# Performance work log

Hardware: AMD Instinct MI355X
Metric: run time of the kernel (lower is better)

The kernel has to match this reference:

```python
import jax, jax.numpy as jnp
import numpy as np

N, IN_F, OUT_F, H = 4096, 256, 64, 8

def setup_inputs() -> dict:
    key = jax.random.key(0)
    k1, k2, k3, k4 = jax.random.split(key, 4)
    x = jax.random.normal(k1, (N, IN_F), dtype=jnp.float32)
    adj = jax.random.randint(k2, (N, N), 0, 2, dtype=jnp.int32)
    # Xavier-uniform-ish init scale for params
    W = jax.random.uniform(k3, (H, IN_F, OUT_F), dtype=jnp.float32, minval=-1.0, maxval=1.0) * np.sqrt(6.0 / (IN_F + OUT_F))
    a = jax.random.uniform(k4, (H, 2 * OUT_F, 1), dtype=jnp.float32, minval=-1.0, maxval=1.0) * np.sqrt(6.0 / (2 * OUT_F + 1))
    return {"x": x, "adj": adj, "W": W, "a": a}

def reference(x, adj, W, a):
    # h: (H, N, F) per-head projected features
    h = jnp.einsum('nf,hfo->hno', x, W)
    F = h.shape[-1]
    # Decompose concat-score: [h_i || h_j] @ a == h_i @ a[:F] + h_j @ a[F:]
    a_src = a[:, :F, 0]   # (H, F)
    a_dst = a[:, F:, 0]   # (H, F)
    src = jnp.einsum('hno,ho->hn', h, a_src)  # (H, N)
    dst = jnp.einsum('hno,ho->hn', h, a_dst)  # (H, N)
    e = jax.nn.leaky_relu(src[:, :, None] + dst[:, None, :], negative_slope=0.2)  # (H, N, N)
    e = jnp.where(adj[None, :, :] == 0, -jnp.inf, e)
    alpha = jax.nn.softmax(e, axis=2)  # dropout is identity at eval
    h_prime = jnp.einsum('hnm,hmo->hno', alpha, h).mean(axis=0)  # (N, F)
    return jax.nn.elu(h_prime)
```

## Files before the change

kernel.cpp:

```cpp
#include <hip/hip_runtime.h>
#include <hip/hip_fp16.h>
#include <cstdint>

#define N_NODES 4096
#define IN_FEAT 256
#define OUT_FEAT 64
#define NHEAD 8
#define LOG2E 1.4426950408889634f

typedef _Float16 f16;
typedef f16   f16x2 __attribute__((ext_vector_type(2)));
typedef f16   f16x8 __attribute__((ext_vector_type(8)));
typedef float f32x4 __attribute__((ext_vector_type(4)));

#define OFF_SRCPK 4194304
#define OFF_DSTE1 4325376
#define OFF_DSTE5 4390912
#define OFF_WT    4456448
#define OFF_EM    4718592
#define OFF_NUMA  21495808ULL
#define OFF_DENA  29884416ULL

union HU { unsigned u; f16x2 h; };
union A8 { f16x8 v; unsigned u[4]; };

__device__ __forceinline__ void async_copy16(const void* g, void* l) {
    __builtin_amdgcn_global_load_lds(
        (const __attribute__((address_space(1))) void*)g,
        (__attribute__((address_space(3))) void*)l, 16, 0, 0);
}

static __device__ inline unsigned pkh2(float a, float b) {
    union { f16 h[2]; unsigned u; } t;
    t.h[0] = (f16)a; t.h[1] = (f16)b; return t.u;
}

__global__ __launch_bounds__(256) void gat_pack(
    const int* __restrict__ adj, unsigned* __restrict__ em32,
    const float* __restrict__ W, f16* __restrict__ Wt,
    float* __restrict__ zeroBase)
{
    if (blockIdx.x >= 1088) {
        size_t off = ((size_t)(blockIdx.x - 1088) * 256 + threadIdx.x) * 8;
        float4 z = {0.f, 0.f, 0.f, 0.f};
        *(float4*)(zeroBase + off)     = z;
        *(float4*)(zeroBase + off + 4) = z;
        return;
    }
    if (blockIdx.x >= 1024) {
        int gid = (blockIdx.x - 1024) * 256 + threadIdx.x;
        int hd  = gid >> 11;
        int rem = gid & 2047;
        int c   = rem >> 5;
        int kg  = rem & 31;
        const float* src = W + ((size_t)hd * IN_FEAT + kg * 8) * OUT_FEAT + c;
        f16x8 v;
        #pragma unroll
        for (int t = 0; t < 8; ++t) v[t] = (f16)src[(size_t)t * OUT_FEAT];
        *(f16x8*)(Wt + ((size_t)hd * OUT_FEAT + c) * IN_FEAT + kg * 8) = v;
        return;
    }

    const int wv   = threadIdx.x >> 6;
    const int lane = threadIdx.x & 63;
    const int row  = blockIdx.x * 4 + wv;
    const int* p   = adj + (size_t)row * N_NODES;
    unsigned* dst  = em32 + (size_t)row * (N_NODES / 4);
    #pragma unroll 4
    for (int s = 0; s < 16; ++s) {
        int4 v = *(const int4*)(p + s * 256 + lane * 4);
        unsigned d = (v.x ? 0x000000FFu : 0u) | (v.y ? 0x0000FF00u : 0u)
                   | (v.z ? 0x00FF0000u : 0u) | (v.w ? 0xFF000000u : 0u);
        dst[s * 64 + lane] = d;
    }
}

__global__ __launch_bounds__(256, 4) void gat_phase1(
    const float* __restrict__ x,
    const f16*   __restrict__ Wt,
    const float* __restrict__ a,
    f16*      __restrict__ h_t,
    unsigned* __restrict__ srcPK,
    f16*      __restrict__ dstE1,
    f16*      __restrict__ dstE5)
{
    __shared__ f16 xs[16][264];

    const int lane = threadIdx.x & 63;
    const int wv   = threadIdx.x >> 6;
    const int tile = blockIdx.x >> 1;
    const int hd   = (blockIdx.x & 1) * 4 + wv;
    const int r    = lane & 15;
    const int q    = lane >> 4;
    const int nb   = tile * 16;

    #pragma unroll
    for (int c = 0; c < 4; ++c) {
        int idx = c * 1024 + threadIdx.x * 4;
        int row = idx >> 8, col = idx & 255;
        float4 v = *(const float4*)(x + (size_t)(nb + row) * IN_FEAT + col);
        uint2 st = { pkh2(v.x, v.y), pkh2(v.z, v.w) };
        *(uint2*)(&xs[row][col]) = st;
    }
    __syncthreads();

    const f16* Wth = Wt + (size_t)hd * OUT_FEAT * IN_FEAT;
    f32x4 acc[4] = {};

    #pragma unroll 2
    for (int k0 = 0; k0 < IN_FEAT; k0 += 32) {
        f16x8 af = *(const f16x8*)(&xs[r][k0 + q * 8]);
        #pragma unroll
        for (int f = 0; f < 4; ++f) {
            f16x8 bf = *(const f16x8*)(Wth + (size_t)(16 * f + r) * IN_FEAT + k0 + q * 8);
            acc[f] = __builtin_amdgcn_mfma_f32_16x16x32_f16(af, bf, acc[f], 0, 0, 0);
        }
    }

    float asv[4], adv[4];
    #pragma unroll
    for (int f = 0; f < 4; ++f) {
        asv[f] = a[hd * 128 + 16 * f + r];
        adv[f] = a[hd * 128 + 64 + 16 * f + r];
    }
    float sp[4], dp[4];
    #pragma unroll
    for (int reg = 0; reg < 4; ++reg) {
        sp[reg] = acc[0][reg] * asv[0] + acc[1][reg] * asv[1]
                + acc[2][reg] * asv[2] + acc[3][reg] * asv[3];
        dp[reg] = acc[0][reg] * adv[0] + acc[1][reg] * adv[1]
                + acc[2][reg] * adv[2] + acc[3][reg] * adv[3];
    }
    #pragma unroll
    for (int m = 1; m <= 8; m <<= 1) {
        #pragma unroll
        for (int reg = 0; reg < 4; ++reg) {
            sp[reg] += __shfl_xor(sp[reg], m);
            dp[reg] += __shfl_xor(dp[reg], m);
        }
    }

    #pragma unroll
    for (int f = 0; f < 4; ++f) {
        uint2 st = { pkh2(acc[f][0], acc[f][1]), pkh2(acc[f][2], acc[f][3]) };
        *(uint2*)(h_t + (size_t)(hd * OUT_FEAT + 16 * f + r) * N_NODES + nb + 4 * q) = st;
    }

    if (r == 0) {
        #pragma unroll
        for (int reg = 0; reg < 4; ++reg) {
            int row = nb + 4 * q + reg;
            float s = sp[reg] * LOG2E;
            float d = dp[reg] * LOG2E;
            srcPK[hd * N_NODES + row] = pkh2(exp2f(s), exp2f(0.2f * s));
            dstE1[hd * N_NODES + row] = (f16)exp2f(d);
            dstE5[hd * N_NODES + row] = (f16)exp2f(0.2f * d);
        }
    }
}

__global__ __launch_bounds__(256, 4) void gat_phase2p(
    const f16* __restrict__ h_t,
    const unsigned* __restrict__ srcPK,
    const f16* __restrict__ dstE1,
    const f16* __restrict__ dstE5,
    const unsigned char* __restrict__ emask8,
    float* __restrict__ numA,
    float* __restrict__ denA)
{
    __shared__ f16 Vbuf[2][8320];

    const int t    = threadIdx.x;
    const int lane = t & 63;
    const int wv   = t >> 6;
    const int r    = lane & 15;
    const int q    = lane >> 4;
    const int q8   = q * 8;

    const int hd     = blockIdx.x >> 7;
    const int rowgrp = (blockIdx.x >> 2) & 31;
    const int chunk  = blockIdx.x & 3;
    const int nblk   = rowgrp * 128;
    const int n0     = nblk + wv * 32;
    const int mbase  = chunk * 1024;

    HU s0u, s1u;
    s0u.u = srcPK[hd * N_NODES + n0 + r];
    s1u.u = srcPK[hd * N_NODES + n0 + 16 + r];
    const f16x2 se1_0 = { s0u.h[0], s0u.h[0] };
    const f16x2 se5_0 = { s0u.h[1], s0u.h[1] };
    const f16x2 se1_1 = { s1u.h[0], s1u.h[0] };
    const f16x2 se5_1 = { s1u.h[1], s1u.h[1] };

    const f16* Vhead = h_t + (size_t)hd * OUT_FEAT * N_NODES + mbase;
    const f16* srcV  = Vhead + (size_t)(t >> 2) * N_NODES + (t & 3) * 8;
    const unsigned char* srcM =
        emask8 + (size_t)(nblk + (t >> 1)) * N_NODES + mbase + (t & 1) * 16;
    const f16* ebase = ((t >> 2) & 1) ? dstE5 : dstE1;
    const f16* esrc  = ebase + (size_t)hd * N_NODES + mbase
                             + (t >> 3) * 32 + (t & 3) * 8;

    f32x4 acc0 = {}, acc1 = {}, acc2 = {}, acc3 = {}, accD0 = {};
    f32x4 acc4 = {}, acc5 = {}, acc6 = {}, acc7 = {}, accD1 = {};
    f16x8 ones;
    #pragma unroll
    for (int j = 0; j < 8; ++j) ones[j] = (f16)1.0f;

    auto stage = [&](int buf, int it) {
        const int c64 = it * 64;
        async_copy16(srcV + c64,      &Vbuf[buf][t * 8]);
        async_copy16(srcV + c64 + 32, &Vbuf[buf][2048 + t * 8]);
        async_copy16(srcM + c64,      &Vbuf[buf][4096 + t * 8]);
        async_copy16(srcM + c64 + 32, &Vbuf[buf][6144 + t * 8]);
        if (t < 16) async_copy16(esrc + c64, &Vbuf[buf][8192 + t * 8]);
    };

    stage(0, 0);

    for (int it = 0; it < 16; ++it) {
        const int cur = it & 1;
        __syncthreads();

        stage(1 - cur, (it + 1) & 15);

        #pragma unroll
        for (int s = 0; s < 2; ++s) {
            const int vb = s * 2048;
            uint4 e1v = *(const uint4*)(&Vbuf[cur][8192 + s * 64 + q8]);
            uint4 e5v = *(const uint4*)(&Vbuf[cur][8224 + s * 64 + q8]);
            uint2 m0v = *(const uint2*)(&Vbuf[cur][4096 + s * 2048 + (wv * 32 + r) * 16 + q * 4]);
            uint2 m1v = *(const uint2*)(&Vbuf[cur][4096 + s * 2048 + (wv * 32 + 16 + r) * 16 + q * 4]);

            unsigned e1d[4] = {e1v.x, e1v.y, e1v.z, e1v.w};
            unsigned e5d[4] = {e5v.x, e5v.y, e5v.z, e5v.w};
            unsigned mk0[4], mk1[4];
            mk0[0] = __builtin_amdgcn_perm(0u, m0v.x, 0x01010000u);
            mk0[1] = __builtin_amdgcn_perm(0u, m0v.x, 0x03030202u);
            mk0[2] = __builtin_amdgcn_perm(0u, m0v.y, 0x01010000u);
            mk0[3] = __builtin_amdgcn_perm(0u, m0v.y, 0x03030202u);
            mk1[0] = __builtin_amdgcn_perm(0u, m1v.x, 0x01010000u);
            mk1[1] = __builtin_amdgcn_perm(0u, m1v.x, 0x03030202u);
            mk1[2] = __builtin_amdgcn_perm(0u, m1v.y, 0x01010000u);
            mk1[3] = __builtin_amdgcn_perm(0u, m1v.y, 0x03030202u);

            A8 A0, A1;
            #pragma unroll
            for (int jp = 0; jp < 4; ++jp) {
                HU ed1; ed1.u = e1d[jp];
                HU ed5; ed5.u = e5d[jp];
                HU w0, w1;
                w0.h = __builtin_elementwise_max(se1_0 * ed1.h, se5_0 * ed5.h);
                w1.h = __builtin_elementwise_max(se1_1 * ed1.h, se5_1 * ed5.h);
                A0.u[jp] = w0.u & mk0[jp];
                A1.u[jp] = w1.u & mk1[jp];
            }

            f16x8 b0 = *(const f16x8*)(&Vbuf[cur][vb + (     r) * 32 + q8]);
            f16x8 b1 = *(const f16x8*)(&Vbuf[cur][vb + (16 + r) * 32 + q8]);
            f16x8 b2 = *(const f16x8*)(&Vbuf[cur][vb + (32 + r) * 32 + q8]);
            f16x8 b3 = *(const f16x8*)(&Vbuf[cur][vb + (48 + r) * 32 + q8]);

            acc0  = __builtin_amdgcn_mfma_f32_16x16x32_f16(A0.v, b0,   acc0,  0, 0, 0);
            acc1  = __builtin_amdgcn_mfma_f32_16x16x32_f16(A0.v, b1,   acc1,  0, 0, 0);
            acc2  = __builtin_amdgcn_mfma_f32_16x16x32_f16(A0.v, b2,   acc2,  0, 0, 0);
            acc3  = __builtin_amdgcn_mfma_f32_16x16x32_f16(A0.v, b3,   acc3,  0, 0, 0);
            accD0 = __builtin_amdgcn_mfma_f32_16x16x32_f16(A0.v, ones, accD0, 0, 0, 0);
            acc4  = __builtin_amdgcn_mfma_f32_16x16x32_f16(A1.v, b0,   acc4,  0, 0, 0);
            acc5  = __builtin_amdgcn_mfma_f32_16x16x32_f16(A1.v, b1,   acc5,  0, 0, 0);
            acc6  = __builtin_amdgcn_mfma_f32_16x16x32_f16(A1.v, b2,   acc6,  0, 0, 0);
            acc7  = __builtin_amdgcn_mfma_f32_16x16x32_f16(A1.v, b3,   acc7,  0, 0, 0);
            accD1 = __builtin_amdgcn_mfma_f32_16x16x32_f16(A1.v, ones, accD1, 0, 0, 0);
        }
    }

    #pragma unroll
    for (int reg = 0; reg < 4; ++reg) {
        int row0 = n0 + 4 * q + reg;
        int row1 = row0 + 16;
        atomicAdd(&numA[((size_t)row0 * NHEAD + hd) * 64 +  0 + r], acc0[reg]);
        atomicAdd(&numA[((size_t)row0 * NHEAD + hd) * 64 + 16 + r], acc1[reg]);
        atomicAdd(&numA[((size_t)row0 * NHEAD + hd) * 64 + 32 + r], acc2[reg]);
        atomicAdd(&numA[((size_t)row0 * NHEAD + hd) * 64 + 48 + r], acc3[reg]);
        atomicAdd(&numA[((size_t)row1 * NHEAD + hd) * 64 +  0 + r], acc4[reg]);
        atomicAdd(&numA[((size_t)row1 * NHEAD + hd) * 64 + 16 + r], acc5[reg]);
        atomicAdd(&numA[((size_t)row1 * NHEAD + hd) * 64 + 32 + r], acc6[reg]);
        atomicAdd(&numA[((size_t)row1 * NHEAD + hd) * 64 + 48 + r], acc7[reg]);
        if (r == 0) {
            atomicAdd(&denA[(size_t)row0 * NHEAD + hd], accD0[reg]);
            atomicAdd(&denA[(size_t)row1 * NHEAD + hd], accD1[reg]);
        }
    }
}

__global__ __launch_bounds__(512) void gat_combine(
    const float* __restrict__ numA,
    const float* __restrict__ denA,
    float* __restrict__ out)
{
    int gid = blockIdx.x * 512 + threadIdx.x;
    int row = gid >> 5;
    int cp  = (gid & 31) * 2;
    float s0 = 0.f, s1 = 0.f;
    #pragma unroll
    for (int h = 0; h < NHEAD; ++h) {
        float2 v = *(const float2*)(numA + ((size_t)row * NHEAD + h) * 64 + cp);
        float inv = 1.f / denA[(size_t)row * NHEAD + h];
        s0 += v.x * inv;
        s1 += v.y * inv;
    }
    s0 *= 0.125f; s1 *= 0.125f;
    float e0 = s0 > 0.f ? s0 : expm1f(s0);
    float e1 = s1 > 0.f ? s1 : expm1f(s1);
    float2 pk = {e0, e1};
    *(float2*)(out + (size_t)row * OUT_FEAT + cp) = pk;
}

extern "C" void kernel_launch(void* const* d_in, const int* in_sizes, int n_in,
                              void* d_out, int out_size, void* d_ws, size_t ws_size,
                              hipStream_t stream)
{
    const float* x   = (const float*)d_in[0];
    const int*   adj = (const int*)d_in[1];
    const float* W   = (const float*)d_in[2];
    const float* a   = (const float*)d_in[3];
    float* out = (float*)d_out;

    char* ws = (char*)d_ws;
    f16*           h_t   = (f16*)ws;
    unsigned*      srcPK = (unsigned*)(ws + OFF_SRCPK);
    f16*           dstE1 = (f16*)(ws + OFF_DSTE1);
    f16*           dstE5 = (f16*)(ws + OFF_DSTE5);
    f16*           Wt    = (f16*)(ws + OFF_WT);
    unsigned char* em    = (unsigned char*)(ws + OFF_EM);
    float*         numA  = (float*)(ws + OFF_NUMA);
    float*         denA  = (float*)(ws + OFF_DENA);

    gat_pack   <<<2128, 256, 0, stream>>>(adj, (unsigned*)em, W, Wt, numA);
    gat_phase1 <<<512,  256, 0, stream>>>(x, Wt, a, h_t, srcPK, dstE1, dstE5);
    gat_phase2p<<<1024, 256, 0, stream>>>(h_t, srcPK, dstE1, dstE5, em, numA, denA);
    gat_combine<<<256,  512, 0, stream>>>(numA, denA, out);
}
```

Baseline: 172.1 us.

## Merge pack and projection kernels, read fp32 W directly in MFMA loop

Fuses the adjacency packing, accumulator zeroing and per-head projection into a single launch, so the separate W transpose/convert pass and its workspace are gone. The projection blocks now gather and convert W from fp32 directly inside the MFMA loop using strided scalar loads. This removes one kernel launch and one dependency boundary, and lets the projection overlap with the bandwidth-bound adjacency packing. The cost is uncoalesced global reads of W, repeated across tiles.

```diff
diff --git a/kernel.cpp b/kernel.cpp
--- a/kernel.cpp
+++ b/kernel.cpp
@@ -16,7 +16,6 @@
 #define OFF_SRCPK 4194304
 #define OFF_DSTE1 4325376
 #define OFF_DSTE5 4390912
-#define OFF_WT    4456448
 #define OFF_EM    4718592
 #define OFF_NUMA  21495808ULL
 #define OFF_DENA  29884416ULL
@@ -35,49 +34,12 @@
     t.h[0] = (f16)a; t.h[1] = (f16)b; return t.u;
 }
 
-__global__ __launch_bounds__(256) void gat_pack(
-    const int* __restrict__ adj, unsigned* __restrict__ em32,
-    const float* __restrict__ W, f16* __restrict__ Wt,
-    float* __restrict__ zeroBase)
-{
-    if (blockIdx.x >= 1088) {
-        size_t off = ((size_t)(blockIdx.x - 1088) * 256 + threadIdx.x) * 8;
-        float4 z = {0.f, 0.f, 0.f, 0.f};
-        *(float4*)(zeroBase + off)     = z;
-        *(float4*)(zeroBase + off + 4) = z;
-        return;
-    }
-    if (blockIdx.x >= 1024) {
-        int gid = (blockIdx.x - 1024) * 256 + threadIdx.x;
-        int hd  = gid >> 11;
-        int rem = gid & 2047;
-        int c   = rem >> 5;
-        int kg  = rem & 31;
-        const float* src = W + ((size_t)hd * IN_FEAT + kg * 8) * OUT_FEAT + c;
-        f16x8 v;
-        #pragma unroll
-        for (int t = 0; t < 8; ++t) v[t] = (f16)src[(size_t)t * OUT_FEAT];
-        *(f16x8*)(Wt + ((size_t)hd * OUT_FEAT + c) * IN_FEAT + kg * 8) = v;
-        return;
-    }
-
-    const int wv   = threadIdx.x >> 6;
-    const int lane = threadIdx.x & 63;
-    const int row  = blockIdx.x * 4 + wv;
-    const int* p   = adj + (size_t)row * N_NODES;
-    unsigned* dst  = em32 + (size_t)row * (N_NODES / 4);
-    #pragma unroll 4
-    for (int s = 0; s < 16; ++s) {
-        int4 v = *(const int4*)(p + s * 256 + lane * 4);
-        unsigned d = (v.x ? 0x000000FFu : 0u) | (v.y ? 0x0000FF00u : 0u)
-                   | (v.z ? 0x00FF0000u : 0u) | (v.w ? 0xFF000000u : 0u);
-        dst[s * 64 + lane] = d;
-    }
-}
-
-__global__ __launch_bounds__(256, 4) void gat_phase1(
+__global__ __launch_bounds__(256, 4) void gat_prep(
+    const int*   __restrict__ adj,
+    unsigned*    __restrict__ em32,
+    float*       __restrict__ zeroBase,
     const float* __restrict__ x,
-    const f16*   __restrict__ Wt,
+    const float* __restrict__ W,
     const float* __restrict__ a,
     f16*      __restrict__ h_t,
     unsigned* __restrict__ srcPK,
@@ -86,6 +48,30 @@
 {
     __shared__ f16 xs[16][264];
 
+    if (blockIdx.x >= 1536) {
+        size_t off = ((size_t)(blockIdx.x - 1536) * 256 + threadIdx.x) * 8;
+        float4 z = {0.f, 0.f, 0.f, 0.f};
+        *(float4*)(zeroBase + off)     = z;
+        *(float4*)(zeroBase + off + 4) = z;
+        return;
+    }
+    if (blockIdx.x >= 512) {
+        const int bi   = blockIdx.x - 512;
+        const int wv   = threadIdx.x >> 6;
+        const int lane = threadIdx.x & 63;
+        const int row  = bi * 4 + wv;
+        const int* p   = adj + (size_t)row * N_NODES;
+        unsigned* dst  = em32 + (size_t)row * (N_NODES / 4);
+        #pragma unroll 4
+        for (int s = 0; s < 16; ++s) {
+            int4 v = *(const int4*)(p + s * 256 + lane * 4);
+            unsigned d = (v.x ? 0x000000FFu : 0u) | (v.y ? 0x0000FF00u : 0u)
+                       | (v.z ? 0x00FF0000u : 0u) | (v.w ? 0xFF000000u : 0u);
+            dst[s * 64 + lane] = d;
+        }
+        return;
+    }
+
     const int lane = threadIdx.x & 63;
     const int wv   = threadIdx.x >> 6;
     const int tile = blockIdx.x >> 1;
@@ -104,7 +90,7 @@
     }
     __syncthreads();
 
-    const f16* Wth = Wt + (size_t)hd * OUT_FEAT * IN_FEAT;
+    const float* Wg = W + (size_t)hd * (IN_FEAT * OUT_FEAT);
     f32x4 acc[4] = {};
 
     #pragma unroll 2
@@ -112,7 +98,10 @@
         f16x8 af = *(const f16x8*)(&xs[r][k0 + q * 8]);
         #pragma unroll
         for (int f = 0; f < 4; ++f) {
-            f16x8 bf = *(const f16x8*)(Wth + (size_t)(16 * f + r) * IN_FEAT + k0 + q * 8);
+            f16x8 bf;
+            #pragma unroll
+            for (int j = 0; j < 8; ++j)
+                bf[j] = (f16)Wg[(size_t)(k0 + q * 8 + j) * OUT_FEAT + 16 * f + r];
             acc[f] = __builtin_amdgcn_mfma_f32_16x16x32_f16(af, bf, acc[f], 0, 0, 0);
         }
     }
@@ -330,13 +319,12 @@
     unsigned*      srcPK = (unsigned*)(ws + OFF_SRCPK);
     f16*           dstE1 = (f16*)(ws + OFF_DSTE1);
     f16*           dstE5 = (f16*)(ws + OFF_DSTE5);
-    f16*           Wt    = (f16*)(ws + OFF_WT);
     unsigned char* em    = (unsigned char*)(ws + OFF_EM);
     float*         numA  = (float*)(ws + OFF_NUMA);
     float*         denA  = (float*)(ws + OFF_DENA);
 
-    gat_pack   <<<2128, 256, 0, stream>>>(adj, (unsigned*)em, W, Wt, numA);
-    gat_phase1 <<<512,  256, 0, stream>>>(x, Wt, a, h_t, srcPK, dstE1, dstE5);
+    gat_prep   <<<2576, 256, 0, stream>>>(adj, (unsigned*)em, numA,
+                                          x, W, a, h_t, srcPK, dstE1, dstE5);
     gat_phase2p<<<1024, 256, 0, stream>>>(h_t, srcPK, dstE1, dstE5, em, numA, denA);
     gat_combine<<<256,  512, 0, stream>>>(numA, denA, out);
 }
```

Result: faster. 165.6 us (-3.8%).
